# Kernel tuning notes

Hardware: AMD Instinct MI355X
Metric: run time of the kernel (lower is better)

The kernel has to match this reference:

```python
import jax, jax.numpy as jnp
import numpy as np

EPS = 1e-5
KF = 3  # kernel_field

def _layernorm(x, g, b):
    m = jnp.mean(x, axis=-1, keepdims=True)
    v = jnp.var(x, axis=-1, keepdims=True)
    return (x - m) * jax.lax.rsqrt(v + EPS) * g + b

def _sai2token(buf, W_mlp):
    # buf: [b, c, a, h, w] -> tokens [h*w, b*a, spa_dim]
    b, c, a, h, w = buf.shape
    x = buf.transpose(0, 2, 1, 3, 4).reshape(b * a, c, h, w)
    xp = jnp.pad(x, ((0, 0), (0, 0), (1, 1), (1, 1)))
    # torch F.unfold ordering: channel slowest, then kernel (i, j)
    patches = jnp.stack([xp[:, :, i:i + h, j:j + w] for i in range(KF) for j in range(KF)], axis=2)
    tok = patches.reshape(b * a, c * KF * KF, h * w).transpose(2, 0, 1)  # [hw, ba, c*9]
    return tok @ W_mlp

def _attention(x, Wqkv, Wproj, bproj, Wl, bl, Ww, bw, lamb, num_heads):
    B, N, C = x.shape
    hd = C // num_heads
    scale = hd ** -0.5
    qkv = (x @ Wqkv).reshape(B, N, 3, num_heads, hd).transpose(2, 0, 3, 1, 4)
    q, k, v = qkv[0] * scale, qkv[1], qkv[2]  # each [B, H, N, hd]
    attn = jnp.einsum('bhnd,bhmd->bhnm', q, k)
    # talking-heads mix before softmax (proj_l)
    attn = jnp.einsum('bhnm,gh->bgnm', attn, Wl) + bl[None, :, None, None]
    attn = jax.nn.softmax(attn, axis=-1)
    # talking-heads mix after softmax (proj_w)
    attn = jnp.einsum('bhnm,gh->bgnm', attn, Ww) + bw[None, :, None, None]
    # attnscale: attn_d + (attn - attn_d) * (1 + lamb_h)
    attn_d = 1.0 / N
    attn = attn_d + (attn - attn_d) * (1.0 + lamb[None, :, None, None])
    out = jnp.einsum('bhnm,bhmd->bhnd', attn, v).transpose(0, 2, 1, 3).reshape(B, N, C)
    return out @ Wproj + bproj


def setup_inputs() -> dict:
    key = jax.random.key(0)
    ks = jax.random.split(key, 20)
    b, c, a, h, w = 4, 128, 25, 32, 32
    D = 2 * c           # spa_dim = 256
    H = 8               # num_heads
    cin = c * KF * KF   # 1152
    f32 = jnp.float32
    def nrm(k, shp, s=0.02):
        return (jax.random.normal(k, shp, dtype=f32) * s)
    return {
        'buffer': jax.random.normal(ks[0], (b, c, a, h, w), dtype=f32),
        'spa_position': jax.random.normal(ks[1], (b, c, a, h, w), dtype=f32) * 0.02,
        'W_mlp': nrm(ks[2], (cin, D)),
        'g1': jnp.ones((D,), f32), 'b1': jnp.zeros((D,), f32),
        'Wqkv': nrm(ks[3], (D, 3 * D)),
        'Wproj': nrm(ks[4], (D, D)), 'bproj': jnp.zeros((D,), f32),
        'Wl': nrm(ks[5], (H, H), 0.3), 'bl': jnp.zeros((H,), f32),
        'Ww': nrm(ks[6], (H, H), 0.3), 'bw': jnp.zeros((H,), f32),
        'lamb': jnp.zeros((H,), f32),
        'g2': jnp.ones((D,), f32), 'b2': jnp.zeros((D,), f32),
        'W1': nrm(ks[7], (D, 2 * D)),
        'W2': nrm(ks[8], (2 * D, D)),
        'Wconv': nrm(ks[9], (c, D)),
    }


def reference(buffer, spa_position, W_mlp, g1, b1, Wqkv, Wproj, bproj,
              Wl, bl, Ww, bw, lamb, g2, b2, W1, W2, Wconv):
    b, c, a, h, w = buffer.shape
    num_heads = Wl.shape[0]
    # gen_mask is computed in the original forward but never used -> omitted.
    spa_token = _sai2token(buffer, W_mlp)          # [hw, ba, D]
    spa_PE = _sai2token(spa_position, W_mlp)       # [hw, ba, D]
    x = _layernorm(spa_token + spa_PE, g1, b1)
    spa_token = _attention(x, Wqkv, Wproj, bproj, Wl, bl, Ww, bw, lamb, num_heads) + spa_token
    # feed-forward: LN -> Linear(D,2D,no bias) -> ReLU -> Linear(2D,D,no bias)
    y = _layernorm(spa_token, g2, b2)
    y = jax.nn.relu(y @ W1) @ W2
    spa_token = y + spa_token
    # Token2SAI: '(h w) (b a) c -> b c a h w' then 1x1x1 Conv3d (D -> c, no bias)
    D = spa_token.shape[-1]
    buf = spa_token.reshape(h, w, b, a, D).transpose(2, 4, 3, 0, 1)  # [b, D, a, h, w]
    out = jnp.einsum('bdahw,od->boahw', buf, Wconv)
    return out
```

## Files before the change

kernel.cpp:

```cpp
#include <hip/hip_runtime.h>
#include <hip/hip_bf16.h>

typedef unsigned short u16;
typedef unsigned int u32;
typedef short bf16x8 __attribute__((ext_vector_type(8)));
typedef float f32x4 __attribute__((ext_vector_type(4)));

#define MFMA(a,b,c) __builtin_amdgcn_mfma_f32_16x16x32_bf16((a),(b),(c),0,0,0)

__device__ __forceinline__ float bf2f(u16 v) { u32 t = ((u32)v) << 16; float f; __builtin_memcpy(&f, &t, 4); return f; }
__device__ __forceinline__ u16 f2bf(float f) { u32 x; __builtin_memcpy(&x, &f, 4); u32 r = (x + 0x7FFFu + ((x >> 16) & 1u)) >> 16; return (u16)r; }
__device__ __forceinline__ float san(float v) { return (fabsf(v) < 1e30f) ? v : 0.f; }
__device__ __forceinline__ float lde(const void* p, long i, int flag) {
    return flag ? bf2f(((const u16*)p)[i]) : ((const float*)p)[i];
}

__device__ __forceinline__ bf16x8 ldfrag8(const u16* p) {
    union { bf16x8 v; uint2 q[2]; } u;
    u.q[0] = *(const uint2*)p;
    u.q[1] = *(const uint2*)(p + 4);
    return u.v;
}
__device__ __forceinline__ bf16x8 ldfrag16(const u16* p) {
    union { bf16x8 v; uint4 q; } u;
    u.q = *(const uint4*)p;
    return u.v;
}

__global__ void detect_dtype(const u32* __restrict__ g1w, int* __restrict__ flag) {
    if (threadIdx.x == 0 && blockIdx.x == 0)
        *flag = (g1w[0] == 0x3F800000u) ? 0 : 1;
}

__global__ __launch_bounds__(256) void fill_sentinel(float* __restrict__ out, int n) {
    int i = blockIdx.x * 256 + threadIdx.x;
    if (i < n) out[i] = 2.0f;
}

__global__ __launch_bounds__(256) void prep_weights(
    const void* __restrict__ Wmlp, const void* __restrict__ Wqkv,
    const void* __restrict__ Wproj, const void* __restrict__ W1,
    const void* __restrict__ W2, const void* __restrict__ Wconv,
    const void* __restrict__ g1, const void* __restrict__ b1,
    const void* __restrict__ g2, const void* __restrict__ b2,
    const void* __restrict__ bproj, const void* __restrict__ Wl,
    const void* __restrict__ Ww, const void* __restrict__ bl,
    const void* __restrict__ bw, const void* __restrict__ lamb,
    u16* __restrict__ Wt1, u16* __restrict__ WqkvT, u16* __restrict__ WprojT,
    u16* __restrict__ W1T, u16* __restrict__ W2T, u16* __restrict__ WconvF,
    float* __restrict__ PRM, const int* __restrict__ flagp)
{
    int i = blockIdx.x * 256 + threadIdx.x;
    int flag = *flagp;
    if (i < 294912) {
        int d = i / 1152, kp = i % 1152;
        int pos9 = kp >> 7, ch = kp & 127;
        Wt1[i] = f2bf(lde(Wmlp, (ch * 9 + pos9) * 256 + d, flag));
    } else if (i < 491520) {
        int j = i - 294912; int jj = j / 256, kk = j % 256;
        WqkvT[j] = f2bf(lde(Wqkv, kk * 768 + jj, flag));
    } else if (i < 557056) {
        int j = i - 491520; int jj = j / 256, kk = j % 256;
        WprojT[j] = f2bf(lde(Wproj, kk * 256 + jj, flag));
    } else if (i < 688128) {
        int j = i - 557056; int jj = j / 256, kk = j % 256;
        W1T[j] = f2bf(lde(W1, kk * 512 + jj, flag));
    } else if (i < 819200) {
        int j = i - 688128; int jj = j / 512, kk = j % 512;
        W2T[j] = f2bf(lde(W2, kk * 256 + jj, flag));
    } else if (i < 851968) {
        int j = i - 819200;
        WconvF[j] = f2bf(lde(Wconv, j, flag));
    } else if (i < 853400) {
        int idx = i - 851968;
        float v;
        if      (idx < 256)  v = lde(g1,    idx,        flag);
        else if (idx < 512)  v = lde(b1,    idx - 256,  flag);
        else if (idx < 768)  v = lde(g2,    idx - 512,  flag);
        else if (idx < 1024) v = lde(b2,    idx - 768,  flag);
        else if (idx < 1280) v = lde(bproj, idx - 1024, flag);
        else if (idx < 1344) v = lde(Wl,    idx - 1280, flag);
        else if (idx < 1408) v = lde(Ww,    idx - 1344, flag);
        else if (idx < 1416) v = lde(bl,    idx - 1408, flag);
        else if (idx < 1424) v = lde(bw,    idx - 1416, flag);
        else                 v = lde(lamb,  idx - 1424, flag);
        PRM[idx] = v;
    }
}

__global__ __launch_bounds__(256) void make_tokens(
    const void* __restrict__ buf, const void* __restrict__ pos,
    u16* __restrict__ tb, u16* __restrict__ ts, const int* __restrict__ flagp)
{
    __shared__ u16 t0[64 * 66];
    __shared__ u16 t1[64 * 66];
    int flag = *flagp;
    int nba = blockIdx.z; int bb = nba / 25, aa = nba % 25;
    int ch0 = blockIdx.y * 64, p0 = blockIdx.x * 64;
    int lane = threadIdx.x & 63, grp = threadIdx.x >> 6;
    for (int cc = grp; cc < 64; cc += 4) {
        long gi = ((long)(bb * 128 + ch0 + cc) * 25 + aa) * 1024 + p0 + lane;
        float v0 = lde(buf, gi, flag);
        float v1 = lde(pos, gi, flag);
        t0[cc * 66 + lane] = f2bf(v0);
        t1[cc * 66 + lane] = f2bf(v0 + v1);
    }
    __syncthreads();
    for (int pp = grp; pp < 64; pp += 4) {
        size_t go = (size_t)(p0 + pp) * 12800 + (size_t)nba * 128 + ch0 + lane;
        tb[go] = t0[lane * 66 + pp];
        ts[go] = t1[lane * 66 + pp];
    }
}

__global__ __launch_bounds__(256) void gemm_conv(
    const u16* __restrict__ Tin, const u16* __restrict__ Wt, u16* __restrict__ C)
{
    __shared__ u16 As[64 * 72];
    __shared__ u16 Bs[64 * 72];
    const int m0 = blockIdx.y * 64, n0 = blockIdx.x * 64;
    const int tid = threadIdx.x;
    const int lane = tid & 63, wave = tid >> 6;
    const int m_off = (wave >> 1) * 32, n_off = (wave & 1) * 32;
    const int l15 = lane & 15, l4 = lane >> 4;
    const int sr = tid >> 2, sk = (tid & 3) * 16;
    const int srow = m0 + sr;
    const int spp = srow / 100, snb = srow % 100;
    const int y = spp >> 5, x = spp & 31;
    f32x4 acc00 = {}, acc01 = {}, acc10 = {}, acc11 = {};
    u16* aw = &As[sr * 72 + sk];
    u16* bw = &Bs[sr * 72 + sk];
    const u16* Bg = Wt + (size_t)(n0 + sr) * 1152 + sk;
    for (int k0 = 0; k0 < 1152; k0 += 64) {
        int pos9 = k0 >> 7;
        int ch = (k0 & 127) + sk;
        int dy = pos9 / 3 - 1, dx = pos9 % 3 - 1;
        int yy = y + dy, xx = x + dx;
        uint4 a0 = {0, 0, 0, 0}, a1 = {0, 0, 0, 0};
        if (yy >= 0 && yy < 32 && xx >= 0 && xx < 32) {
            const u16* src = Tin + ((size_t)(yy * 32 + xx) * 100 + snb) * 128 + ch;
            a0 = *(const uint4*)src;
            a1 = *(const uint4*)(src + 8);
        }
        uint4 b0 = *(const uint4*)(Bg + k0);
        uint4 b1 = *(const uint4*)(Bg + k0 + 8);
        __syncthreads();
        uint2* ap = (uint2*)aw; uint2 t;
        t.x = a0.x; t.y = a0.y; ap[0] = t;
        t.x = a0.z; t.y = a0.w; ap[1] = t;
        t.x = a1.x; t.y = a1.y; ap[2] = t;
        t.x = a1.z; t.y = a1.w; ap[3] = t;
        uint2* bp = (uint2*)bw;
        t.x = b0.x; t.y = b0.y; bp[0] = t;
        t.x = b0.z; t.y = b0.w; bp[1] = t;
        t.x = b1.x; t.y = b1.y; bp[2] = t;
        t.x = b1.z; t.y = b1.w; bp[3] = t;
        __syncthreads();
#pragma unroll
        for (int ks = 0; ks < 2; ++ks) {
            const int kb = ks * 32 + l4 * 8;
            bf16x8 af0 = ldfrag8(&As[(m_off + l15) * 72 + kb]);
            bf16x8 af1 = ldfrag8(&As[(m_off + 16 + l15) * 72 + kb]);
            bf16x8 bf0 = ldfrag8(&Bs[(n_off + l15) * 72 + kb]);
            bf16x8 bf1 = ldfrag8(&Bs[(n_off + 16 + l15) * 72 + kb]);
            acc00 = MFMA(af0, bf0, acc00);
            acc01 = MFMA(af0, bf1, acc01);
            acc10 = MFMA(af1, bf0, acc10);
            acc11 = MFMA(af1, bf1, acc11);
        }
    }
    f32x4 accs[2][2] = {{acc00, acc01}, {acc10, acc11}};
#pragma unroll
    for (int i = 0; i < 2; ++i)
#pragma unroll
        for (int j = 0; j < 2; ++j) {
            int col = n0 + n_off + j * 16 + l15;
#pragma unroll
            for (int r = 0; r < 4; ++r) {
                int row = m0 + m_off + i * 16 + l4 * 4 + r;
                C[(size_t)row * 256 + col] = f2bf(san(accs[i][j][r]));
            }
        }
}

template<int MODE>
__global__ __launch_bounds__(256) void gemm_bt(
    const u16* __restrict__ A, const u16* __restrict__ Bt, u16* __restrict__ C,
    int M, int N, int K,
    const float* __restrict__ bias, const u16* __restrict__ res,
    float* __restrict__ Cf)
{
    __shared__ u16 As[64 * 72];
    __shared__ u16 Bs[64 * 72];
    const int m0 = blockIdx.y * 64, n0 = blockIdx.x * 64;
    const int tid = threadIdx.x;
    const int lane = tid & 63, wave = tid >> 6;
    const int m_off = (wave >> 1) * 32, n_off = (wave & 1) * 32;
    const int l15 = lane & 15, l4 = lane >> 4;
    const int sr = tid >> 2, sk = (tid & 3) * 16;
    f32x4 acc00 = {}, acc01 = {}, acc10 = {}, acc11 = {};
    const u16* Ag = A + (size_t)(m0 + sr) * K + sk;
    const u16* Bg = Bt + (size_t)(n0 + sr) * K + sk;
    u16* aw = &As[sr * 72 + sk];
    u16* bw = &Bs[sr * 72 + sk];
    for (int k0 = 0; k0 < K; k0 += 64) {
        uint4 a0 = *(const uint4*)(Ag + k0);
        uint4 a1 = *(const uint4*)(Ag + k0 + 8);
        uint4 b0 = *(const uint4*)(Bg + k0);
        uint4 b1 = *(const uint4*)(Bg + k0 + 8);
        __syncthreads();
        uint2* ap = (uint2*)aw; uint2 t;
        t.x = a0.x; t.y = a0.y; ap[0] = t;
        t.x = a0.z; t.y = a0.w; ap[1] = t;
        t.x = a1.x; t.y = a1.y; ap[2] = t;
        t.x = a1.z; t.y = a1.w; ap[3] = t;
        uint2* bp = (uint2*)bw;
        t.x = b0.x; t.y = b0.y; bp[0] = t;
        t.x = b0.z; t.y = b0.w; bp[1] = t;
        t.x = b1.x; t.y = b1.y; bp[2] = t;
        t.x = b1.z; t.y = b1.w; bp[3] = t;
        __syncthreads();
#pragma unroll
        for (int ks = 0; ks < 2; ++ks) {
            const int kb = ks * 32 + l4 * 8;
            bf16x8 af0 = ldfrag8(&As[(m_off + l15) * 72 + kb]);
            bf16x8 af1 = ldfrag8(&As[(m_off + 16 + l15) * 72 + kb]);
            bf16x8 bf0 = ldfrag8(&Bs[(n_off + l15) * 72 + kb]);
            bf16x8 bf1 = ldfrag8(&Bs[(n_off + 16 + l15) * 72 + kb]);
            acc00 = MFMA(af0, bf0, acc00);
            acc01 = MFMA(af0, bf1, acc01);
            acc10 = MFMA(af1, bf0, acc10);
            acc11 = MFMA(af1, bf1, acc11);
        }
    }
    f32x4 accs[2][2] = {{acc00, acc01}, {acc10, acc11}};
#pragma unroll
    for (int i = 0; i < 2; ++i)
#pragma unroll
        for (int j = 0; j < 2; ++j) {
            int col = n0 + n_off + j * 16 + l15;
#pragma unroll
            for (int r = 0; r < 4; ++r) {
                int row = m0 + m_off + i * 16 + l4 * 4 + r;
                float v = san(accs[i][j][r]);
                if (MODE == 0) {
                    C[(size_t)row * N + col] = f2bf(v);
                } else if (MODE == 1) {
                    v += bias[col] + bf2f(res[(size_t)row * N + col]);
                    C[(size_t)row * N + col] = f2bf(san(v));
                } else if (MODE == 2) {
                    C[(size_t)row * N + col] = f2bf(fmaxf(v, 0.f));
                } else if (MODE == 3) {
                    v += bf2f(res[(size_t)row * N + col]);
                    int pp = row / 100, nb = row % 100;
                    C[((size_t)nb * 1024 + pp) * 256 + col] = f2bf(san(v));
                } else {
                    int nb = col >> 10, pp = col & 1023;
                    int bb = nb / 25, aa = nb % 25;
                    Cf[(((size_t)bb * 128 + row) * 25 + aa) * 1024 + pp] = v;
                }
            }
        }
}

__global__ __launch_bounds__(256) void ln_kernel(
    const u16* __restrict__ in, const float* __restrict__ g,
    const float* __restrict__ b, u16* __restrict__ out)
{
    int wave = threadIdx.x >> 6, lane = threadIdx.x & 63;
    size_t row = (size_t)blockIdx.x * 4 + wave;
    const u16* rp = in + row * 256 + lane * 4;
    uint2 rv = *(const uint2*)rp;
    float x0 = bf2f(rv.x & 0xffff), x1 = bf2f(rv.x >> 16);
    float x2 = bf2f(rv.y & 0xffff), x3 = bf2f(rv.y >> 16);
    float s = x0 + x1 + x2 + x3;
    float ss = x0 * x0 + x1 * x1 + x2 * x2 + x3 * x3;
    for (int off = 32; off > 0; off >>= 1) { s += __shfl_xor(s, off); ss += __shfl_xor(ss, off); }
    float mean = s * (1.f / 256.f);
    float var = ss * (1.f / 256.f) - mean * mean;
    float inv = rsqrtf(fmaxf(var, 0.f) + 1e-5f);
    float4 gv = *(const float4*)(g + lane * 4);
    float4 bv = *(const float4*)(b + lane * 4);
    u16 o0 = f2bf(san((x0 - mean) * inv * gv.x + bv.x));
    u16 o1 = f2bf(san((x1 - mean) * inv * gv.y + bv.y));
    u16 o2 = f2bf(san((x2 - mean) * inv * gv.z + bv.z));
    u16 o3 = f2bf(san((x3 - mean) * inv * gv.w + bv.w));
    uint2 ov; ov.x = (u32)o0 | ((u32)o1 << 16); ov.y = (u32)o2 | ((u32)o3 << 16);
    *(uint2*)(out + row * 256 + lane * 4) = ov;
}

__global__ __launch_bounds__(256) void attn_fused(
    const u16* __restrict__ qkv, const float* __restrict__ prm,
    u16* __restrict__ AO)
{
    const int MSS = 104;
    const int MSV = 104;
    __shared__ u16 S4s[128 * 104];
    __shared__ u16 vT[256 * 104];
    __shared__ float cl_s[64], ww_s[64];
    __shared__ float bl_s[8], bw_s[8], lam_s[8];
    int p = blockIdx.x;
    int tid = threadIdx.x;
    int lane = tid & 63, wave = tid >> 6;
    int l15 = lane & 15, l4 = lane >> 4;
    if (tid < 64) { cl_s[tid] = prm[1280 + tid] * 0.17677669529663687f; ww_s[tid] = prm[1344 + tid]; }
    else if (tid < 72) { int j = tid - 64; bl_s[j] = prm[1408 + j]; bw_s[j] = prm[1416 + j]; lam_s[j] = prm[1424 + j]; }
    const u16* base = qkv + (size_t)p * 76800;

    {
        int mg = tid >> 5;
        int dv0 = (tid & 31) * 8;
        int rot = tid & 7;
        for (int mb = 0; mb < 100; mb += 8) {
            int m = mb + mg;
            if (m < 100) {
                union { uint4 q; u16 e[8]; } u;
                u.q = *(const uint4*)(base + 512 + (size_t)m * 768 + dv0);
#pragma unroll
                for (int j = 0; j < 8; ++j) {
                    int jj = (j + rot) & 7;
                    vT[(dv0 + jj) * MSV + m] = u.e[jj];
                }
            }
        }
        for (int i = tid; i < 256 * 4; i += 256)
            vT[(i >> 2) * MSV + 100 + (i & 3)] = 0;
    }
    __syncthreads();

    for (int t = 0; t < 7; ++t) {
        int n0 = t * 16;
        int nq = n0 + l15; if (nq > 99) nq = 99;
        bf16x8 qf[8];
#pragma unroll
        for (int h = 0; h < 8; ++h)
            qf[h] = ldfrag16(base + nq * 768 + h * 32 + l4 * 8);

        for (int u = wave; u < 7; u += 4) {
            int m0 = u * 16;
            int mk = m0 + l15; if (mk > 99) mk = 99;
            f32x4 S[8];
#pragma unroll
            for (int h = 0; h < 8; ++h) {
                bf16x8 kf = ldfrag16(base + mk * 768 + 256 + h * 32 + l4 * 8);
                f32x4 z = {};
                S[h] = MFMA(qf[h], kf, z);
            }
            int mm = m0 + l15;
            if (mm < 100) {
#pragma unroll
                for (int g = 0; g < 8; ++g) {
                    float bgl = bl_s[g];
#pragma unroll
                    for (int r = 0; r < 4; ++r) {
                        float s2 = bgl;
#pragma unroll
                        for (int h = 0; h < 8; ++h) s2 += cl_s[g * 8 + h] * S[h][r];
                        s2 = fminf(fmaxf(s2, -80.f), 80.f);
                        S4s[(g * 16 + l4 * 4 + r) * MSS + mm] = f2bf(s2);
                    }
                }
            }
        }
        __syncthreads();

        {
            int row = tid >> 1, sub = tid & 1;
            u16* rp = S4s + row * MSS + sub * 52;
            float v[52];
#pragma unroll
            for (int i = 0; i < 13; ++i) {
                uint2 d = *(const uint2*)(rp + i * 4);
                v[i * 4 + 0] = bf2f((u16)(d.x & 0xffff));
                v[i * 4 + 1] = bf2f((u16)(d.x >> 16));
                v[i * 4 + 2] = bf2f((u16)(d.y & 0xffff));
                v[i * 4 + 3] = bf2f((u16)(d.y >> 16));
            }
            if (sub) { v[48] = -1e30f; v[49] = -1e30f; v[50] = -1e30f; v[51] = -1e30f; }
            float m0 = v[0], m1 = v[1], m2 = v[2], m3 = v[3];
#pragma unroll
            for (int j = 4; j < 52; j += 4) {
                m0 = fmaxf(m0, v[j]);     m1 = fmaxf(m1, v[j + 1]);
                m2 = fmaxf(m2, v[j + 2]); m3 = fmaxf(m3, v[j + 3]);
            }
            float mx = fmaxf(fmaxf(m0, m1), fmaxf(m2, m3));
            mx = fmaxf(mx, __shfl_xor(mx, 1));
            float s0 = 0.f, s1 = 0.f, s2 = 0.f, s3 = 0.f;
#pragma unroll
            for (int j = 0; j < 52; j += 4) {
                v[j]     = __expf(v[j]     - mx); s0 += v[j];
                v[j + 1] = __expf(v[j + 1] - mx); s1 += v[j + 1];
                v[j + 2] = __expf(v[j + 2] - mx); s2 += v[j + 2];
                v[j + 3] = __expf(v[j + 3] - mx); s3 += v[j + 3];
            }
            float sum = (s0 + s1) + (s2 + s3);
            sum += __shfl_xor(sum, 1);
            float inv = 1.f / sum;
#pragma unroll
            for (int i = 0; i < 13; ++i) {
                uint2 d;
                d.x = (u32)f2bf(v[i * 4 + 0] * inv) | ((u32)f2bf(v[i * 4 + 1] * inv) << 16);
                d.y = (u32)f2bf(v[i * 4 + 2] * inv) | ((u32)f2bf(v[i * 4 + 3] * inv) << 16);
                *(uint2*)(rp + i * 4) = d;
            }
        }
        __syncthreads();

        for (int idx = tid; idx < 832; idx += 256) {
            int nl = idx / 52, mc = idx - (idx / 52) * 52;
            float P0[8], P1[8];
#pragma unroll
            for (int g = 0; g < 8; ++g) {
                u32 d = *(const u32*)&S4s[(g * 16 + nl) * MSS + mc * 2];
                P0[g] = bf2f((u16)(d & 0xffff));
                P1[g] = bf2f((u16)(d >> 16));
            }
#pragma unroll
            for (int gp = 0; gp < 8; ++gp) {
                float a = bw_s[gp], b = bw_s[gp];
#pragma unroll
                for (int g = 0; g < 8; ++g) {
                    float w = ww_s[gp * 8 + g];
                    a += w * P0[g]; b += w * P1[g];
                }
                float lg = 1.f + lam_s[gp];
                a = 0.01f + (a - 0.01f) * lg;
                b = 0.01f + (b - 0.01f) * lg;
                u32 d = (u32)f2bf(san(a)) | ((u32)f2bf(san(b)) << 16);
                *(u32*)&S4s[(gp * 16 + nl) * MSS + mc * 2] = d;
            }
        }
        __syncthreads();

        {
            bf16x8 zz = {};
#pragma unroll
            for (int gi = 0; gi < 2; ++gi) {
                int g = wave * 2 + gi;
                bf16x8 pa[4];
#pragma unroll
                for (int ks = 0; ks < 3; ++ks)
                    pa[ks] = ldfrag8(&S4s[(g * 16 + l15) * MSS + ks * 32 + l4 * 8]);
                pa[3] = (l4 == 0) ? ldfrag8(&S4s[(g * 16 + l15) * MSS + 96]) : zz;
#pragma unroll
                for (int dh = 0; dh < 2; ++dh) {
                    int vd = g * 32 + dh * 16 + l15;
                    f32x4 acc = {};
#pragma unroll
                    for (int ks = 0; ks < 3; ++ks) {
                        bf16x8 vb = ldfrag8(&vT[vd * MSV + ks * 32 + l4 * 8]);
                        acc = MFMA(pa[ks], vb, acc);
                    }
                    bf16x8 vb3 = (l4 == 0) ? ldfrag8(&vT[vd * MSV + 96]) : zz;
                    acc = MFMA(pa[3], vb3, acc);
#pragma unroll
                    for (int r = 0; r < 4; ++r) {
                        int n = n0 + l4 * 4 + r;
                        if (n < 100)
                            AO[((size_t)p * 100 + n) * 256 + g * 32 + dh * 16 + l15] = f2bf(san(acc[r]));
                    }
                }
            }
        }
        __syncthreads();
    }
}

extern "C" void kernel_launch(void* const* d_in, const int* in_sizes, int n_in,
                              void* d_out, int out_size, void* d_ws, size_t ws_size,
                              hipStream_t stream) {
    (void)in_sizes; (void)n_in;
    const void* buffer  = d_in[0];
    const void* spa_pos = d_in[1];
    const void* W_mlp   = d_in[2];
    const void* g1      = d_in[3];
    const void* b1      = d_in[4];
    const void* Wqkv    = d_in[5];
    const void* Wproj   = d_in[6];
    const void* bproj   = d_in[7];
    const void* Wl      = d_in[8];
    const void* bl      = d_in[9];
    const void* Ww      = d_in[10];
    const void* bw      = d_in[11];
    const void* lamb    = d_in[12];
    const void* g2      = d_in[13];
    const void* b2      = d_in[14];
    const void* W1      = d_in[15];
    const void* W2      = d_in[16];
    const void* Wconv   = d_in[17];

    if (ws_size < 263856132ULL) {
        fill_sentinel<<<(out_size + 255) / 256, 256, 0, stream>>>((float*)d_out, out_size);
        return;
    }

    char* ws = (char*)d_ws;
    u16* TINB  = (u16*)(ws + 0);
    u16* TINS  = (u16*)(ws + 26214400);
    u16* X     = (u16*)(ws + 0);
    u16* AO    = (u16*)(ws + 0);
    u16* Y0    = (u16*)(ws + 0);
    u16* T0    = (u16*)(ws + 52428800);
    u16* SPA3  = (u16*)(ws + 52428800);
    u16* T1    = (u16*)(ws + 104857600);
    u16* QKV   = (u16*)(ws + 104857600);
    u16* SPA2  = (u16*)(ws + 104857600);
    u16* H1    = (u16*)(ws + 157286400);
    u16* WT1   = (u16*)(ws + 262144000);
    u16* WQKVT = (u16*)(ws + 262733824);
    u16* WPROJT= (u16*)(ws + 263127040);
    u16* W1T   = (u16*)(ws + 263258112);
    u16* W2T   = (u16*)(ws + 263520256);
    u16* WCONVF= (u16*)(ws + 263782400);
    float* PRM = (float*)(ws + 263847936);
    int* FLAG  = (int*)(ws + 263856128);

    detect_dtype<<<1, 64, 0, stream>>>((const u32*)g1, FLAG);
    prep_weights<<<3334, 256, 0, stream>>>(W_mlp, Wqkv, Wproj, W1, W2, Wconv,
                                           g1, b1, g2, b2, bproj, Wl, Ww, bl, bw, lamb,
                                           WT1, WQKVT, WPROJT, W1T, W2T, WCONVF, PRM, FLAG);
    make_tokens<<<dim3(16, 2, 100), 256, 0, stream>>>(buffer, spa_pos, TINB, TINS, FLAG);
    gemm_conv<<<dim3(4, 1600), 256, 0, stream>>>(TINB, WT1, T0);
    gemm_conv<<<dim3(4, 1600), 256, 0, stream>>>(TINS, WT1, T1);
    ln_kernel<<<25600, 256, 0, stream>>>(T1, PRM + 0, PRM + 256, X);
    gemm_bt<0><<<dim3(12, 1600), 256, 0, stream>>>(X, WQKVT, QKV, 102400, 768, 256, nullptr, nullptr, nullptr);
    attn_fused<<<1024, 256, 0, stream>>>(QKV, PRM, AO);
    gemm_bt<1><<<dim3(4, 1600), 256, 0, stream>>>(AO, WPROJT, SPA2, 102400, 256, 256, PRM + 1024, T0, nullptr);
    ln_kernel<<<25600, 256, 0, stream>>>(SPA2, PRM + 512, PRM + 768, Y0);
    gemm_bt<2><<<dim3(8, 1600), 256, 0, stream>>>(Y0, W1T, H1, 102400, 512, 256, nullptr, nullptr, nullptr);
    gemm_bt<3><<<dim3(4, 1600), 256, 0, stream>>>(H1, W2T, SPA3, 102400, 256, 512, nullptr, SPA2, nullptr);
    gemm_bt<4><<<dim3(1600, 2), 256, 0, stream>>>(WCONVF, SPA3, nullptr, 128, 102400, 256, nullptr, nullptr, (float*)d_out);
}
```

Baseline: 1.043 ms.

## Use 128x128 GEMM tiles with direct global-to-LDS loads

All GEMM kernels, including the implicit-im2col conv GEMM, move from 64x64 to 128x128 block tiles with a 4x4 MFMA accumulator grid per wave. Tiles are staged with global_load_lds, which writes global memory straight into shared memory instead of going through registers. Out-of-bounds conv taps now read from a small zero buffer in the workspace. The goal is higher operand reuse and fewer instructions per MFMA, at the cost of more accumulator registers, an unpadded LDS layout that may cause bank conflicts, and no double buffering.

```diff
diff --git a/kernel.cpp b/kernel.cpp
--- a/kernel.cpp
+++ b/kernel.cpp
@@ -25,6 +25,12 @@
     union { bf16x8 v; uint4 q; } u;
     u.q = *(const uint4*)p;
     return u.v;
+}
+
+__device__ __forceinline__ void gload16(const u16* g, u16* l) {
+    __builtin_amdgcn_global_load_lds(
+        (const __attribute__((address_space(1))) u16*)g,
+        (__attribute__((address_space(3))) u16*)l, 16, 0, 0);
 }
 
 __global__ void detect_dtype(const u32* __restrict__ g1w, int* __restrict__ flag) {
@@ -48,7 +54,7 @@
     const void* __restrict__ bw, const void* __restrict__ lamb,
     u16* __restrict__ Wt1, u16* __restrict__ WqkvT, u16* __restrict__ WprojT,
     u16* __restrict__ W1T, u16* __restrict__ W2T, u16* __restrict__ WconvF,
-    float* __restrict__ PRM, const int* __restrict__ flagp)
+    float* __restrict__ PRM, u16* __restrict__ ZEROB, const int* __restrict__ flagp)
 {
     int i = blockIdx.x * 256 + threadIdx.x;
     int flag = *flagp;
@@ -85,6 +91,8 @@
         else if (idx < 1424) v = lde(bw,    idx - 1416, flag);
         else                 v = lde(lamb,  idx - 1424, flag);
         PRM[idx] = v;
+    } else if (i < 853464) {
+        ZEROB[i - 853400] = 0;
     }
 }
 
@@ -114,71 +122,77 @@
 }
 
 __global__ __launch_bounds__(256) void gemm_conv(
-    const u16* __restrict__ Tin, const u16* __restrict__ Wt, u16* __restrict__ C)
+    const u16* __restrict__ Tin, const u16* __restrict__ Wt, u16* __restrict__ C,
+    const u16* __restrict__ ZB)
 {
-    __shared__ u16 As[64 * 72];
-    __shared__ u16 Bs[64 * 72];
-    const int m0 = blockIdx.y * 64, n0 = blockIdx.x * 64;
+    __shared__ u16 As[128 * 64];
+    __shared__ u16 Bs[128 * 64];
+    const int m0 = blockIdx.y * 128, n0 = blockIdx.x * 128;
     const int tid = threadIdx.x;
     const int lane = tid & 63, wave = tid >> 6;
-    const int m_off = (wave >> 1) * 32, n_off = (wave & 1) * 32;
+    const int wr = wave >> 1, wc = wave & 1;
     const int l15 = lane & 15, l4 = lane >> 4;
-    const int sr = tid >> 2, sk = (tid & 3) * 16;
-    const int srow = m0 + sr;
-    const int spp = srow / 100, snb = srow % 100;
-    const int y = spp >> 5, x = spp & 31;
-    f32x4 acc00 = {}, acc01 = {}, acc10 = {}, acc11 = {};
-    u16* aw = &As[sr * 72 + sk];
-    u16* bw = &Bs[sr * 72 + sk];
-    const u16* Bg = Wt + (size_t)(n0 + sr) * 1152 + sk;
-    for (int k0 = 0; k0 < 1152; k0 += 64) {
-        int pos9 = k0 >> 7;
-        int ch = (k0 & 127) + sk;
+    const int colk = (tid & 7) * 8;
+    int ys[4], xs[4];
+    const u16* Ab[4];
+#pragma unroll
+    for (int i = 0; i < 4; ++i) {
+        int row = m0 + i * 32 + (tid >> 3);
+        int pp = row / 100, snb = row - pp * 100;
+        ys[i] = pp >> 5; xs[i] = pp & 31;
+        Ab[i] = Tin + (size_t)snb * 128 + colk;
+    }
+    const u16* Bg = Wt + (size_t)(n0 + (tid >> 3)) * 1152 + colk;
+    u16* Asw = &As[(wave * 8) * 64];
+    u16* Bsw = &Bs[(wave * 8) * 64];
+    f32x4 acc[4][4] = {};
+
+    auto stage = [&](int k0) {
+        int pos9 = k0 >> 7, ch0 = k0 & 127;
         int dy = pos9 / 3 - 1, dx = pos9 % 3 - 1;
-        int yy = y + dy, xx = x + dx;
-        uint4 a0 = {0, 0, 0, 0}, a1 = {0, 0, 0, 0};
-        if (yy >= 0 && yy < 32 && xx >= 0 && xx < 32) {
-            const u16* src = Tin + ((size_t)(yy * 32 + xx) * 100 + snb) * 128 + ch;
-            a0 = *(const uint4*)src;
-            a1 = *(const uint4*)(src + 8);
-        }
-        uint4 b0 = *(const uint4*)(Bg + k0);
-        uint4 b1 = *(const uint4*)(Bg + k0 + 8);
-        __syncthreads();
-        uint2* ap = (uint2*)aw; uint2 t;
-        t.x = a0.x; t.y = a0.y; ap[0] = t;
-        t.x = a0.z; t.y = a0.w; ap[1] = t;
-        t.x = a1.x; t.y = a1.y; ap[2] = t;
-        t.x = a1.z; t.y = a1.w; ap[3] = t;
-        uint2* bp = (uint2*)bw;
-        t.x = b0.x; t.y = b0.y; bp[0] = t;
-        t.x = b0.z; t.y = b0.w; bp[1] = t;
-        t.x = b1.x; t.y = b1.y; bp[2] = t;
-        t.x = b1.z; t.y = b1.w; bp[3] = t;
+#pragma unroll
+        for (int i = 0; i < 4; ++i) {
+            int yy = ys[i] + dy, xx = xs[i] + dx;
+            bool ok = ((unsigned)yy < 32u) && ((unsigned)xx < 32u);
+            const u16* src = ok ? (Ab[i] + (size_t)(yy * 32 + xx) * 12800 + ch0) : ZB;
+            gload16(src, Asw + i * 32 * 64);
+            gload16(Bg + (size_t)i * 32 * 1152 + k0, Bsw + i * 32 * 64);
+        }
+    };
+
+    stage(0);
+    int k0 = 0;
+    while (true) {
         __syncthreads();
 #pragma unroll
         for (int ks = 0; ks < 2; ++ks) {
-            const int kb = ks * 32 + l4 * 8;
-            bf16x8 af0 = ldfrag8(&As[(m_off + l15) * 72 + kb]);
-            bf16x8 af1 = ldfrag8(&As[(m_off + 16 + l15) * 72 + kb]);
-            bf16x8 bf0 = ldfrag8(&Bs[(n_off + l15) * 72 + kb]);
-            bf16x8 bf1 = ldfrag8(&Bs[(n_off + 16 + l15) * 72 + kb]);
-            acc00 = MFMA(af0, bf0, acc00);
-            acc01 = MFMA(af0, bf1, acc01);
-            acc10 = MFMA(af1, bf0, acc10);
-            acc11 = MFMA(af1, bf1, acc11);
-        }
-    }
-    f32x4 accs[2][2] = {{acc00, acc01}, {acc10, acc11}};
-#pragma unroll
-    for (int i = 0; i < 2; ++i)
-#pragma unroll
-        for (int j = 0; j < 2; ++j) {
-            int col = n0 + n_off + j * 16 + l15;
+            const int koff = ks * 32 + l4 * 8;
+            bf16x8 af[4], bq[4];
+#pragma unroll
+            for (int q = 0; q < 4; ++q) {
+                af[q] = ldfrag16(&As[(wr * 64 + q * 16 + l15) * 64 + koff]);
+                bq[q] = ldfrag16(&Bs[(wc * 64 + q * 16 + l15) * 64 + koff]);
+            }
+#pragma unroll
+            for (int mi = 0; mi < 4; ++mi)
+#pragma unroll
+                for (int ni = 0; ni < 4; ++ni)
+                    acc[mi][ni] = MFMA(af[mi], bq[ni], acc[mi][ni]);
+        }
+        k0 += 64;
+        if (k0 >= 1152) break;
+        __syncthreads();
+        stage(k0);
+    }
+#pragma unroll
+    for (int mi = 0; mi < 4; ++mi)
+#pragma unroll
+        for (int ni = 0; ni < 4; ++ni) {
+            int col = n0 + wc * 64 + ni * 16 + l15;
 #pragma unroll
             for (int r = 0; r < 4; ++r) {
-                int row = m0 + m_off + i * 16 + l4 * 4 + r;
-                C[(size_t)row * 256 + col] = f2bf(san(accs[i][j][r]));
+                int row = m0 + wr * 64 + mi * 16 + l4 * 4 + r;
+                C[(size_t)row * 256 + col] = f2bf(san(acc[mi][ni][r]));
             }
         }
 }
@@ -190,59 +204,61 @@
     const float* __restrict__ bias, const u16* __restrict__ res,
     float* __restrict__ Cf)
 {
-    __shared__ u16 As[64 * 72];
-    __shared__ u16 Bs[64 * 72];
-    const int m0 = blockIdx.y * 64, n0 = blockIdx.x * 64;
+    __shared__ u16 As[128 * 64];
+    __shared__ u16 Bs[128 * 64];
+    const int m0 = blockIdx.y * 128, n0 = blockIdx.x * 128;
     const int tid = threadIdx.x;
     const int lane = tid & 63, wave = tid >> 6;
-    const int m_off = (wave >> 1) * 32, n_off = (wave & 1) * 32;
+    const int wr = wave >> 1, wc = wave & 1;
     const int l15 = lane & 15, l4 = lane >> 4;
-    const int sr = tid >> 2, sk = (tid & 3) * 16;
-    f32x4 acc00 = {}, acc01 = {}, acc10 = {}, acc11 = {};
-    const u16* Ag = A + (size_t)(m0 + sr) * K + sk;
-    const u16* Bg = Bt + (size_t)(n0 + sr) * K + sk;
-    u16* aw = &As[sr * 72 + sk];
-    u16* bw = &Bs[sr * 72 + sk];
-    for (int k0 = 0; k0 < K; k0 += 64) {
-        uint4 a0 = *(const uint4*)(Ag + k0);
-        uint4 a1 = *(const uint4*)(Ag + k0 + 8);
-        uint4 b0 = *(const uint4*)(Bg + k0);
-        uint4 b1 = *(const uint4*)(Bg + k0 + 8);
-        __syncthreads();
-        uint2* ap = (uint2*)aw; uint2 t;
-        t.x = a0.x; t.y = a0.y; ap[0] = t;
-        t.x = a0.z; t.y = a0.w; ap[1] = t;
-        t.x = a1.x; t.y = a1.y; ap[2] = t;
-        t.x = a1.z; t.y = a1.w; ap[3] = t;
-        uint2* bp = (uint2*)bw;
-        t.x = b0.x; t.y = b0.y; bp[0] = t;
-        t.x = b0.z; t.y = b0.w; bp[1] = t;
-        t.x = b1.x; t.y = b1.y; bp[2] = t;
-        t.x = b1.z; t.y = b1.w; bp[3] = t;
+    const u16* Ag = A + (size_t)(m0 + (tid >> 3)) * K + (tid & 7) * 8;
+    const u16* Bg = Bt + (size_t)(n0 + (tid >> 3)) * K + (tid & 7) * 8;
+    u16* Asw = &As[(wave * 8) * 64];
+    u16* Bsw = &Bs[(wave * 8) * 64];
+    const size_t rstep = (size_t)32 * K;
+    f32x4 acc[4][4] = {};
+
+#pragma unroll
+    for (int i = 0; i < 4; ++i) {
+        gload16(Ag + (size_t)i * rstep, Asw + i * 32 * 64);
+        gload16(Bg + (size_t)i * rstep, Bsw + i * 32 * 64);
+    }
+    int k0 = 0;
+    while (true) {
         __syncthreads();
 #pragma unroll
         for (int ks = 0; ks < 2; ++ks) {
-            const int kb = ks * 32 + l4 * 8;
-            bf16x8 af0 = ldfrag8(&As[(m_off + l15) * 72 + kb]);
-            bf16x8 af1 = ldfrag8(&As[(m_off + 16 + l15) * 72 + kb]);
-            bf16x8 bf0 = ldfrag8(&Bs[(n_off + l15) * 72 + kb]);
-            bf16x8 bf1 = ldfrag8(&Bs[(n_off + 16 + l15) * 72 + kb]);
-            acc00 = MFMA(af0, bf0, acc00);
-            acc01 = MFMA(af0, bf1, acc01);
-            acc10 = MFMA(af1, bf0, acc10);
-            acc11 = MFMA(af1, bf1, acc11);
-        }
-    }
-    f32x4 accs[2][2] = {{acc00, acc01}, {acc10, acc11}};
-#pragma unroll
-    for (int i = 0; i < 2; ++i)
-#pragma unroll
-        for (int j = 0; j < 2; ++j) {
-            int col = n0 + n_off + j * 16 + l15;
+            const int koff = ks * 32 + l4 * 8;
+            bf16x8 af[4], bq[4];
+#pragma unroll
+            for (int q = 0; q < 4; ++q) {
+                af[q] = ldfrag16(&As[(wr * 64 + q * 16 + l15) * 64 + koff]);
+                bq[q] = ldfrag16(&Bs[(wc * 64 + q * 16 + l15) * 64 + koff]);
+            }
+#pragma unroll
+            for (int mi = 0; mi < 4; ++mi)
+#pragma unroll
+                for (int ni = 0; ni < 4; ++ni)
+                    acc[mi][ni] = MFMA(af[mi], bq[ni], acc[mi][ni]);
+        }
+        k0 += 64;
+        if (k0 >= K) break;
+        __syncthreads();
+#pragma unroll
+        for (int i = 0; i < 4; ++i) {
+            gload16(Ag + k0 + (size_t)i * rstep, Asw + i * 32 * 64);
+            gload16(Bg + k0 + (size_t)i * rstep, Bsw + i * 32 * 64);
+        }
+    }
+#pragma unroll
+    for (int mi = 0; mi < 4; ++mi)
+#pragma unroll
+        for (int ni = 0; ni < 4; ++ni) {
+            int col = n0 + wc * 64 + ni * 16 + l15;
 #pragma unroll
             for (int r = 0; r < 4; ++r) {
-                int row = m0 + m_off + i * 16 + l4 * 4 + r;
-                float v = san(accs[i][j][r]);
+                int row = m0 + wr * 64 + mi * 16 + l4 * 4 + r;
+                float v = san(acc[mi][ni][r]);
                 if (MODE == 0) {
                     C[(size_t)row * N + col] = f2bf(v);
                 } else if (MODE == 1) {
@@ -489,7 +505,7 @@
     const void* W2      = d_in[16];
     const void* Wconv   = d_in[17];
 
-    if (ws_size < 263856132ULL) {
+    if (ws_size < 263856320ULL) {
         fill_sentinel<<<(out_size + 255) / 256, 256, 0, stream>>>((float*)d_out, out_size);
         return;
     }
@@ -514,20 +530,21 @@
     u16* WCONVF= (u16*)(ws + 263782400);
     float* PRM = (float*)(ws + 263847936);
     int* FLAG  = (int*)(ws + 263856128);
+    u16* ZB    = (u16*)(ws + 263856192);
 
     detect_dtype<<<1, 64, 0, stream>>>((const u32*)g1, FLAG);
     prep_weights<<<3334, 256, 0, stream>>>(W_mlp, Wqkv, Wproj, W1, W2, Wconv,
                                            g1, b1, g2, b2, bproj, Wl, Ww, bl, bw, lamb,
-                                           WT1, WQKVT, WPROJT, W1T, W2T, WCONVF, PRM, FLAG);
+                                           WT1, WQKVT, WPROJT, W1T, W2T, WCONVF, PRM, ZB, FLAG);
     make_tokens<<<dim3(16, 2, 100), 256, 0, stream>>>(buffer, spa_pos, TINB, TINS, FLAG);
-    gemm_conv<<<dim3(4, 1600), 256, 0, stream>>>(TINB, WT1, T0);
-    gemm_conv<<<dim3(4, 1600), 256, 0, stream>>>(TINS, WT1, T1);
+    gemm_conv<<<dim3(2, 800), 256, 0, stream>>>(TINB, WT1, T0, ZB);
+    gemm_conv<<<dim3(2, 800), 256, 0, stream>>>(TINS, WT1, T1, ZB);
     ln_kernel<<<25600, 256, 0, stream>>>(T1, PRM + 0, PRM + 256, X);
-    gemm_bt<0><<<dim3(12, 1600), 256, 0, stream>>>(X, WQKVT, QKV, 102400, 768, 256, nullptr, nullptr, nullptr);
+    gemm_bt<0><<<dim3(6, 800), 256, 0, stream>>>(X, WQKVT, QKV, 102400, 768, 256, nullptr, nullptr, nullptr);
     attn_fused<<<1024, 256, 0, stream>>>(QKV, PRM, AO);
-    gemm_bt<1><<<dim3(4, 1600), 256, 0, stream>>>(AO, WPROJT, SPA2, 102400, 256, 256, PRM + 1024, T0, nullptr);
+    gemm_bt<1><<<dim3(2, 800), 256, 0, stream>>>(AO, WPROJT, SPA2, 102400, 256, 256, PRM + 1024, T0, nullptr);
     ln_kernel<<<25600, 256, 0, stream>>>(SPA2, PRM + 512, PRM + 768, Y0);
-    gemm_bt<2><<<dim3(8, 1600), 256, 0, stream>>>(Y0, W1T, H1, 102400, 512, 256, nullptr, nullptr, nullptr);
-    gemm_bt<3><<<dim3(4, 1600), 256, 0, stream>>>(H1, W2T, SPA3, 102400, 256, 512, nullptr, SPA2, nullptr);
-    gemm_bt<4><<<dim3(1600, 2), 256, 0, stream>>>(WCONVF, SPA3, nullptr, 128, 102400, 256, nullptr, nullptr, (float*)d_out);
-}
+    gemm_bt<2><<<dim3(4, 800), 256, 0, stream>>>(Y0, W1T, H1, 102400, 512, 256, nullptr, nullptr, nullptr);
+    gemm_bt<3><<<dim3(2, 800), 256, 0, stream>>>(H1, W2T, SPA3, 102400, 256, 512, nullptr, SPA2, nullptr);
+    gemm_bt<4><<<dim3(800, 1), 256, 0, stream>>>(WCONVF, SPA3, nullptr, 128, 102400, 256, nullptr, nullptr, (float*)d_out);
+}
```

Measured after the change: 934.3 us. -10.4%, faster.
